# Performance work log

Measured on AMD Instinct MI355X. Metric: run time of the kernel, lower is better.

## Reference

```python
import jax, jax.numpy as jnp
import numpy as np

B, L, D, H, NB = 256, 200, 128, 4, 2
ITEMS = 50000
EPS = 1e-8
C = 0.001
REG = 0.0001


def _ln(x, g, b):
    m = x.mean(-1, keepdims=True)
    v = ((x - m) ** 2).mean(-1, keepdims=True)
    return (x - m) / jnp.sqrt(v + EPS) * g + b


def _mha(q_in, kv_in, in_w, in_b, out_w, out_b, mask):
    # q_in, kv_in: (B, L, D); torch MultiheadAttention math (batch-layout equivalent)
    Wq, Wk, Wv = jnp.split(in_w, 3, axis=0)
    bq, bk, bv = jnp.split(in_b, 3, axis=0)
    hd = D // H
    heads = lambda x: x.reshape(B, L, H, hd).transpose(0, 2, 1, 3)
    q = heads(q_in @ Wq.T + bq)
    k = heads(kv_in @ Wk.T + bk)
    v = heads(kv_in @ Wv.T + bv)
    scores = jnp.einsum('bhqd,bhkd->bhqk', q, k) * (1.0 / np.sqrt(hd))
    scores = jnp.where(mask, -jnp.inf, scores)
    a = jax.nn.softmax(scores, axis=-1)
    o = jnp.einsum('bhqk,bhkd->bhqd', a, v).transpose(0, 2, 1, 3).reshape(B, L, D)
    return o @ out_w.T + out_b


def _log2feats(log_seqs, item_emb, pos_emb, blocks):
    seqs = item_emb[log_seqs]                                   # (B,L,D)
    poss = jnp.arange(1, L + 1)[None, :] * (log_seqs != 0)      # 0 at padding
    seqs = seqs + pos_emb[poss]
    mask = ~jnp.tril(jnp.ones((L, L), dtype=bool))              # causal
    for i in range(NB):
        (ln1_g, ln1_b, in_w, in_b, out_w, out_b,
         ln2_g, ln2_b, c1_w, c1_b, c2_w, c2_b) = [p[i] for p in blocks]
        Q = _ln(seqs, ln1_g, ln1_b)
        seqs = Q + _mha(Q, seqs, in_w, in_b, out_w, out_b, mask)  # residual on Q (as in source)
        seqs = _ln(seqs, ln2_g, ln2_b)
        # PointWiseFeedForward: conv1d k=1 == linear over feature dim, residual add
        seqs = seqs + (jax.nn.relu(seqs @ c1_w.T + c1_b) @ c2_w.T + c2_b)
    return seqs


def setup_inputs() -> dict:
    key = jax.random.key(0)
    ks = jax.random.split(key, 20)
    inp = {
        'user_ids': jax.random.randint(ks[0], (B,), 0, 10000),
        'log_seqs': jax.random.randint(ks[1], (B, L), 0, ITEMS + 1),
        'pos_seqs': jax.random.randint(ks[2], (B, L), 0, ITEMS + 1),
        'item_emb': (jax.random.normal(ks[3], (ITEMS + 1, D)) * 0.02).at[0].set(0.0),
        'pos_emb': (jax.random.normal(ks[4], (L + 1, D)) * 0.02).at[0].set(0.0),
        'pred_w': jax.random.normal(ks[5], (1, D)) * 0.05,
        'ln1_g': jnp.ones((NB, D)), 'ln1_b': jnp.zeros((NB, D)),
        'in_w': jax.random.normal(ks[6], (NB, 3 * D, D)) * 0.05,
        'in_b': jnp.zeros((NB, 3 * D)),
        'out_w': jax.random.normal(ks[7], (NB, D, D)) * 0.05,
        'out_b': jnp.zeros((NB, D)),
        'ln2_g': jnp.ones((NB, D)), 'ln2_b': jnp.zeros((NB, D)),
        'c1_w': jax.random.normal(ks[8], (NB, D, D)) * 0.05,
        'c1_b': jnp.zeros((NB, D)),
        'c2_w': jax.random.normal(ks[9], (NB, D, D)) * 0.05,
        'c2_b': jnp.zeros((NB, D)),
    }
    return inp


def reference(user_ids, log_seqs, pos_seqs, item_emb, pos_emb, pred_w,
              ln1_g, ln1_b, in_w, in_b, out_w, out_b, ln2_g, ln2_b,
              c1_w, c1_b, c2_w, c2_b):
    blocks = (ln1_g, ln1_b, in_w, in_b, out_w, out_b, ln2_g, ln2_b, c1_w, c1_b, c2_w, c2_b)
    F = _log2feats(log_seqs, item_emb, pos_emb, blocks)          # (B,L,D)
    # left: FF = sum_s F F^T (per batch), EE = E^T E over full catalog, hh = w^T w
    FF = jnp.einsum('bsd,bse->bde', F, F)                        # (B,D,D)
    EE = item_emb.T @ item_emb                                   # (D,D)
    hh = pred_w.T @ pred_w                                       # (D,D)
    left = jnp.einsum('bde,ef,fg->b', FF, C * EE, hh)            # sum of FF @ cEE @ hh
    # right: R_hat = h^T (F * q_i)
    pos_e = item_emb[pos_seqs]                                   # (B,L,D)
    R = jnp.einsum('d,bsd->bs', pred_w[0], F * pos_e)
    right = ((1.0 - C) * R ** 2 - 2.0 * R).sum(axis=-1)
    reg = jnp.sqrt((item_emb ** 2).sum())                        # Frobenius norm
    loss = left + right + REG * reg
    return loss.mean()
```

## Files before the change

### kernel.cpp

```cpp
#include <hip/hip_runtime.h>
#include <math.h>

#define B_ 256
#define L_ 200
#define D_ 128
#define H_ 4
#define HD_ 32
#define NB_ 2
#define NROWS (B_ * L_)
#define NITEMS 50001
#define EPS_ 1e-8f
#define C_ 0.001f
#define REG_ 0.0001f

typedef __bf16 bf16x8 __attribute__((ext_vector_type(8)));
typedef short  short8 __attribute__((ext_vector_type(8)));
typedef float  f32x4  __attribute__((ext_vector_type(4)));
typedef unsigned short us4 __attribute__((ext_vector_type(4)));

static __device__ __forceinline__ void split2(float f, unsigned short& h, unsigned short& l) {
  unsigned u = __builtin_bit_cast(unsigned, f);
  unsigned hb = (u + 0x7FFFu + ((u >> 16) & 1u)) >> 16;
  float fl = f - __builtin_bit_cast(float, hb << 16);
  h = (unsigned short)hb;
  l = (unsigned short)(__builtin_bit_cast(unsigned, fl) >> 16);
}

static __device__ __forceinline__ bf16x8 pack8(const unsigned short* s) {
  short8 v;
#pragma unroll
  for (int j = 0; j < 8; ++j) v[j] = (short)s[j];
  return __builtin_bit_cast(bf16x8, v);
}

__global__ __launch_bounds__(256) void k_convw(const float* __restrict__ in_w,
                                               const float* __restrict__ out_w,
                                               const float* __restrict__ c1_w,
                                               const float* __restrict__ c2_w,
                                               unsigned short* __restrict__ Wh,
                                               unsigned short* __restrict__ Wl) {
  int i = (blockIdx.x * 256 + threadIdx.x) * 4;
  if (i >= 196608) return;
  const float* s; int j;
  if (i < 98304)       { s = in_w;  j = i; }
  else if (i < 131072) { s = out_w; j = i - 98304; }
  else if (i < 163840) { s = c1_w;  j = i - 131072; }
  else                 { s = c2_w;  j = i - 163840; }
  float4 v = *(const float4*)(s + j);
  float vf[4] = {v.x, v.y, v.z, v.w};
  us4 hv, lv;
#pragma unroll
  for (int t = 0; t < 4; ++t) {
    unsigned short h, l; split2(vf[t], h, l);
    hv[t] = h; lv[t] = l;
  }
  *(us4*)(Wh + i) = hv;
  *(us4*)(Wl + i) = lv;
}

__global__ __launch_bounds__(256) void k_embed(const int* __restrict__ logs,
                                               const float* __restrict__ item_emb,
                                               const float* __restrict__ pos_emb,
                                               float* __restrict__ X) {
  int gid = blockIdx.x * 256 + threadIdx.x;
  if (gid >= NROWS * 32) return;
  int row = gid >> 5;
  int c4  = (gid & 31) << 2;
  int it  = logs[row];
  int l   = row % L_;
  int pos = (it != 0) ? (l + 1) : 0;
  float4 e = *(const float4*)(item_emb + (size_t)it * D_ + c4);
  float4 p = *(const float4*)(pos_emb + (size_t)pos * D_ + c4);
  float4 o; o.x = e.x + p.x; o.y = e.y + p.y; o.z = e.z + p.z; o.w = e.w + p.w;
  *(float4*)(X + (size_t)row * D_ + c4) = o;
}

__global__ __launch_bounds__(256) void k_ln(const float* __restrict__ in,
                                            const float* __restrict__ g,
                                            const float* __restrict__ bb,
                                            float* __restrict__ out) {
  int wid = threadIdx.x >> 6, lane = threadIdx.x & 63;
  int row = blockIdx.x * 4 + wid;
  float2 x = *(const float2*)(in + (size_t)row * D_ + lane * 2);
  float s = x.x + x.y;
#pragma unroll
  for (int o = 1; o < 64; o <<= 1) s += __shfl_xor(s, o, 64);
  float m = s * (1.f / D_);
  float d0 = x.x - m, d1 = x.y - m;
  float ss = d0 * d0 + d1 * d1;
#pragma unroll
  for (int o = 1; o < 64; o <<= 1) ss += __shfl_xor(ss, o, 64);
  float rs = 1.f / sqrtf(ss * (1.f / D_) + EPS_);
  float2 gv = *(const float2*)(g + lane * 2);
  float2 bv = *(const float2*)(bb + lane * 2);
  float2 o2; o2.x = d0 * rs * gv.x + bv.x; o2.y = d1 * rs * gv.y + bv.y;
  *(float2*)(out + (size_t)row * D_ + lane * 2) = o2;
}

__global__ __launch_bounds__(256) void k_gemm2(const float* __restrict__ A, int lda,
                                               const unsigned short* __restrict__ Wh,
                                               const unsigned short* __restrict__ Wl,
                                               const float* __restrict__ bias,
                                               const float* __restrict__ Res,
                                               float* __restrict__ Cmat, int ldc,
                                               int col0, int epi) {
  Wh   += (size_t)blockIdx.y * 128 * 128;
  Wl   += (size_t)blockIdx.y * 128 * 128;
  bias += blockIdx.y * 128;
  col0 += blockIdx.y * 128;
  __shared__ unsigned short Ah[64][136], Al[64][136];
  const int tid  = threadIdx.x;
  const int bm   = blockIdx.x * 64;
  const int lane = tid & 63, wid = tid >> 6;
  const int n0   = wid * 32;
  const int fr   = lane & 15;
  const int fg   = lane >> 4;

  bf16x8 wh[2][4], wl[2][4];
#pragma unroll
  for (int f = 0; f < 2; f++)
#pragma unroll
    for (int ks = 0; ks < 4; ks++) {
      const unsigned short* p = Wh + (size_t)(n0 + f * 16 + fr) * 128 + ks * 32 + fg * 8;
      const unsigned short* q = Wl + (size_t)(n0 + f * 16 + fr) * 128 + ks * 32 + fg * 8;
      wh[f][ks] = __builtin_bit_cast(bf16x8, *(const short8*)p);
      wl[f][ks] = __builtin_bit_cast(bf16x8, *(const short8*)q);
    }

#pragma unroll
  for (int it = 0; it < 4; ++it) {
    int flat = it * 2048 + tid * 8;
    int r = flat >> 7, c = flat & 127;
    const float* ap = A + (size_t)(bm + r) * lda + c;
    float4 a0 = *(const float4*)ap;
    float4 a1 = *(const float4*)(ap + 4);
    float af[8] = {a0.x, a0.y, a0.z, a0.w, a1.x, a1.y, a1.z, a1.w};
    unsigned short hh[8], ll[8];
#pragma unroll
    for (int j = 0; j < 8; ++j) split2(af[j], hh[j], ll[j]);
    *(short8*)&Ah[r][c] = __builtin_bit_cast(short8, pack8(hh));
    *(short8*)&Al[r][c] = __builtin_bit_cast(short8, pack8(ll));
  }
  __syncthreads();

  f32x4 acc[4][2];
#pragma unroll
  for (int m = 0; m < 4; m++)
#pragma unroll
    for (int f = 0; f < 2; f++) acc[m][f] = (f32x4){0.f, 0.f, 0.f, 0.f};

#pragma unroll
  for (int m = 0; m < 4; m++) {
#pragma unroll
    for (int ks = 0; ks < 4; ks++) {
      bf16x8 ah = *(const bf16x8*)&Ah[m * 16 + fr][ks * 32 + fg * 8];
      bf16x8 al = *(const bf16x8*)&Al[m * 16 + fr][ks * 32 + fg * 8];
#pragma unroll
      for (int f = 0; f < 2; f++) {
        acc[m][f] = __builtin_amdgcn_mfma_f32_16x16x32_bf16(ah, wl[f][ks], acc[m][f], 0, 0, 0);
        acc[m][f] = __builtin_amdgcn_mfma_f32_16x16x32_bf16(al, wh[f][ks], acc[m][f], 0, 0, 0);
        acc[m][f] = __builtin_amdgcn_mfma_f32_16x16x32_bf16(ah, wh[f][ks], acc[m][f], 0, 0, 0);
      }
    }
  }

#pragma unroll
  for (int f = 0; f < 2; f++) {
    int n = n0 + f * 16 + fr;
    float bv = bias[n];
#pragma unroll
    for (int m = 0; m < 4; m++) {
#pragma unroll
      for (int i = 0; i < 4; i++) {
        int row = bm + m * 16 + fg * 4 + i;
        float v = acc[m][f][i] + bv;
        if (epi == 2)      v = fmaxf(v, 0.f);
        else if (epi == 1) v += Res[(size_t)row * D_ + n];
        Cmat[(size_t)row * ldc + col0 + n] = v;
      }
    }
  }
}

__global__ __launch_bounds__(256) void k_attn(const float* __restrict__ qkv,
                                              float* __restrict__ Oq) {
  __shared__ float ks[L_][HD_];
  __shared__ float vs[L_][HD_];
  int b = blockIdx.x >> 2;
  int h = blockIdx.x & 3;
  int tid = threadIdx.x;
  for (int idx = tid; idx < L_ * HD_; idx += 256) {
    int j = idx >> 5, d = idx & 31;
    size_t base = ((size_t)(b * L_ + j)) * 384 + 128 + h * HD_ + d;
    ks[j][d] = qkv[base];
    vs[j][d] = qkv[base + 128];
  }
  __syncthreads();
  int t = tid;
  if (t >= L_) return;
  float q[HD_];
  const float* qp = qkv + ((size_t)(b * L_ + t)) * 384 + h * HD_;
#pragma unroll
  for (int d4 = 0; d4 < HD_; d4 += 4) {
    float4 v = *(const float4*)(qp + d4);
    q[d4] = v.x; q[d4 + 1] = v.y; q[d4 + 2] = v.z; q[d4 + 3] = v.w;
  }
  float o[HD_];
#pragma unroll
  for (int d = 0; d < HD_; d++) o[d] = 0.f;
  float mrun = -INFINITY, lrun = 0.f;
  const float scale = 0.17677669529663687f;
  for (int j = 0; j <= t; j++) {
    float s = 0.f;
#pragma unroll
    for (int d = 0; d < HD_; d++) s += q[d] * ks[j][d];
    s *= scale;
    float mn = fmaxf(mrun, s);
    float corr = __expf(mrun - mn);
    float p = __expf(s - mn);
    lrun = lrun * corr + p;
#pragma unroll
    for (int d = 0; d < HD_; d++) o[d] = o[d] * corr + p * vs[j][d];
    mrun = mn;
  }
  float inv = 1.f / lrun;
  float* op = Oq + ((size_t)(b * L_ + t)) * 384 + h * HD_;
#pragma unroll
  for (int d4 = 0; d4 < HD_; d4 += 4) {
    float4 v;
    v.x = o[d4] * inv; v.y = o[d4 + 1] * inv;
    v.z = o[d4 + 2] * inv; v.w = o[d4 + 3] * inv;
    *(float4*)(op + d4) = v;
  }
}

__global__ void k_zero(float* __restrict__ w_raw, float* __restrict__ reg_sq) {
  int t = threadIdx.x;
  if (t < 128) w_raw[t] = 0.f;
  if (t == 128) reg_sq[0] = 0.f;
}

__global__ __launch_bounds__(256) void k_wreg(const float* __restrict__ item_emb,
                                              const float* __restrict__ pred_w,
                                              float* __restrict__ w_raw,
                                              float* __restrict__ reg_sq) {
  int gw = (blockIdx.x * 256 + threadIdx.x) >> 6;
  int lane = threadIdx.x & 63;
  float2 p2 = *(const float2*)(pred_w + lane * 2);
  float ax = 0.f, ay = 0.f, ssq = 0.f;
  for (int r = gw; r < NITEMS; r += 1024) {
    float2 e = *(const float2*)(item_emb + (size_t)r * D_ + lane * 2);
    float dp = e.x * p2.x + e.y * p2.y;
#pragma unroll
    for (int o = 1; o < 64; o <<= 1) dp += __shfl_xor(dp, o, 64);
    ax += e.x * dp; ay += e.y * dp;
    ssq += e.x * e.x + e.y * e.y;
  }
  atomicAdd(&w_raw[lane * 2 + 0], ax);
  atomicAdd(&w_raw[lane * 2 + 1], ay);
#pragma unroll
  for (int o = 1; o < 64; o <<= 1) ssq += __shfl_xor(ssq, o, 64);
  if (lane == 0) atomicAdd(reg_sq, ssq);
}

__global__ void k_scale(const float* __restrict__ pred_w,
                        const float* __restrict__ w_raw,
                        const float* __restrict__ reg_sq,
                        float* __restrict__ wt, float* __restrict__ out) {
  int t = threadIdx.x;
  __shared__ float sp[128];
  sp[t] = pred_w[t];
  __syncthreads();
  float S = 0.f;
  for (int i = 0; i < 128; i++) S += sp[i];
  wt[t] = C_ * S * w_raw[t];
  if (t == 0) out[0] = REG_ * sqrtf(reg_sq[0]);
}

__global__ __launch_bounds__(256) void k_final(const float* __restrict__ F,
                                               const int* __restrict__ pos_seqs,
                                               const float* __restrict__ item_emb,
                                               const float* __restrict__ pred_w,
                                               const float* __restrict__ wt,
                                               float* __restrict__ out) {
  int b = blockIdx.x;
  int wid = threadIdx.x >> 6, lane = threadIdx.x & 63;
  float2 wt2 = *(const float2*)(wt + lane * 2);
  float2 p2  = *(const float2*)(pred_w + lane * 2);
  float acc = 0.f;
  for (int s = wid; s < L_; s += 4) {
    float2 f = *(const float2*)(F + ((size_t)(b * L_ + s)) * D_ + lane * 2);
    int pi = pos_seqs[b * L_ + s];
    float2 pe = *(const float2*)(item_emb + (size_t)pi * D_ + lane * 2);
    float rsum = f.x + f.y;
    float dw = f.x * wt2.x + f.y * wt2.y;
    float rr = p2.x * f.x * pe.x + p2.y * f.y * pe.y;
#pragma unroll
    for (int o = 1; o < 64; o <<= 1) {
      rsum += __shfl_xor(rsum, o, 64);
      dw   += __shfl_xor(dw, o, 64);
      rr   += __shfl_xor(rr, o, 64);
    }
    acc += rsum * dw + (1.f - C_) * rr * rr - 2.f * rr;
  }
  if (lane == 0) atomicAdd(out, acc * (1.f / B_));
}

extern "C" void kernel_launch(void* const* d_in, const int* in_sizes, int n_in,
                              void* d_out, int out_size, void* d_ws, size_t ws_size,
                              hipStream_t stream) {
  const int*   log_seqs = (const int*)d_in[1];
  const int*   pos_seqs = (const int*)d_in[2];
  const float* item_emb = (const float*)d_in[3];
  const float* pos_emb  = (const float*)d_in[4];
  const float* pred_w   = (const float*)d_in[5];
  const float* ln1_g = (const float*)d_in[6];
  const float* ln1_b = (const float*)d_in[7];
  const float* in_w  = (const float*)d_in[8];
  const float* in_b  = (const float*)d_in[9];
  const float* out_w = (const float*)d_in[10];
  const float* out_b = (const float*)d_in[11];
  const float* ln2_g = (const float*)d_in[12];
  const float* ln2_b = (const float*)d_in[13];
  const float* c1_w  = (const float*)d_in[14];
  const float* c1_b  = (const float*)d_in[15];
  const float* c2_w  = (const float*)d_in[16];
  const float* c2_b  = (const float*)d_in[17];
  float* out = (float*)d_out;

  char* ws = (char*)d_ws;
  const size_t UNIT = (size_t)NROWS * D_ * sizeof(float);
  float* X     = (float*)ws; ws += UNIT;
  float* QB    = (float*)ws; ws += UNIT;
  float* QKV   = (float*)ws; ws += 3 * UNIT;
  unsigned short* WH = (unsigned short*)ws; ws += 196608 * 2;
  unsigned short* WL = (unsigned short*)ws; ws += 196608 * 2;
  float* w_raw = (float*)ws; ws += 512;
  float* wt    = (float*)ws; ws += 512;
  float* reg_sq= (float*)ws; ws += 512;
  if (ws_size < 5 * UNIT + 4 * 196608 + 4096) return;

  const size_t OFF_OUT = 98304, OFF_C1 = 131072, OFF_C2 = 163840;

  k_zero<<<1, 256, 0, stream>>>(w_raw, reg_sq);
  k_convw<<<192, 256, 0, stream>>>(in_w, out_w, c1_w, c2_w, WH, WL);
  k_embed<<<(NROWS * 32) / 256, 256, 0, stream>>>(log_seqs, item_emb, pos_emb, X);

  for (int i = 0; i < NB_; i++) {
    const size_t iwo = (size_t)i * 384 * 128;
    const size_t sqo = (size_t)i * 128 * 128;
    const float* ib = in_b + (size_t)i * 384;
    k_ln<<<NROWS / 4, 256, 0, stream>>>(X, ln1_g + i * 128, ln1_b + i * 128, QB);
    k_gemm2<<<dim3(NROWS / 64, 1), 256, 0, stream>>>(QB, 128, WH + iwo, WL + iwo,
                                                     ib, nullptr, QKV, 384, 0, 0);
    k_gemm2<<<dim3(NROWS / 64, 2), 256, 0, stream>>>(X, 128, WH + iwo + 128 * 128,
                                                     WL + iwo + 128 * 128,
                                                     ib + 128, nullptr, QKV, 384, 128, 0);
    k_attn<<<B_ * H_, 256, 0, stream>>>(QKV, QKV);
    k_gemm2<<<dim3(NROWS / 64, 1), 256, 0, stream>>>(QKV, 384, WH + OFF_OUT + sqo,
                                                     WL + OFF_OUT + sqo,
                                                     out_b + i * 128, QB, X, 128, 0, 1);
    k_ln<<<NROWS / 4, 256, 0, stream>>>(X, ln2_g + i * 128, ln2_b + i * 128, QB);
    k_gemm2<<<dim3(NROWS / 64, 1), 256, 0, stream>>>(QB, 128, WH + OFF_C1 + sqo,
                                                     WL + OFF_C1 + sqo,
                                                     c1_b + i * 128, nullptr, QKV, 128, 0, 2);
    k_gemm2<<<dim3(NROWS / 64, 1), 256, 0, stream>>>(QKV, 128, WH + OFF_C2 + sqo,
                                                     WL + OFF_C2 + sqo,
                                                     c2_b + i * 128, QB, X, 128, 0, 1);
  }

  k_wreg<<<256, 256, 0, stream>>>(item_emb, pred_w, w_raw, reg_sq);
  k_scale<<<1, 128, 0, stream>>>(pred_w, w_raw, reg_sq, wt, out);
  k_final<<<B_, 256, 0, stream>>>(X, pos_seqs, item_emb, pred_w, wt, out);
}
```

Baseline: 786.9 us.

## Rewrite causal attention with split-bf16 MFMA for QK^T and PV

Replaces the per-thread scalar online-softmax attention with a wave-tiled version. K and V are split into bf16 hi/lo pairs in shared memory, with V stored transposed. Scores and the P·V product are computed with three-term 16x16x32 bf16 MFMAs, and softmax runs over causal 16-row tiles using wave shuffles. This removes the scalar FMA-bound inner loop and the load imbalance across causal rows, at the cost of extra split/shuffle work and some precision loss from dropping the lo*lo term.

```diff
diff --git a/kernel.cpp b/kernel.cpp
--- a/kernel.cpp
+++ b/kernel.cpp
@@ -5,13 +5,14 @@
 #define L_ 200
 #define D_ 128
 #define H_ 4
-#define HD_ 32
 #define NB_ 2
 #define NROWS (B_ * L_)
 #define NITEMS 50001
 #define EPS_ 1e-8f
 #define C_ 0.001f
 #define REG_ 0.0001f
+#define KPADK_ 208
+#define KPADV_ 224
 
 typedef __bf16 bf16x8 __attribute__((ext_vector_type(8)));
 typedef short  short8 __attribute__((ext_vector_type(8)));
@@ -182,55 +183,137 @@
   }
 }
 
-__global__ __launch_bounds__(256) void k_attn(const float* __restrict__ qkv,
-                                              float* __restrict__ Oq) {
-  __shared__ float ks[L_][HD_];
-  __shared__ float vs[L_][HD_];
-  int b = blockIdx.x >> 2;
-  int h = blockIdx.x & 3;
-  int tid = threadIdx.x;
-  for (int idx = tid; idx < L_ * HD_; idx += 256) {
-    int j = idx >> 5, d = idx & 31;
-    size_t base = ((size_t)(b * L_ + j)) * 384 + 128 + h * HD_ + d;
-    ks[j][d] = qkv[base];
-    vs[j][d] = qkv[base + 128];
+__global__ __launch_bounds__(256) void k_attn2(const float* __restrict__ qkv,
+                                               float* __restrict__ Oq) {
+  __shared__ unsigned short Kh[KPADK_][32], Kl[KPADK_][32];
+  __shared__ unsigned short Vh[32][KPADV_], Vl[32][KPADV_];
+  const int b = blockIdx.x >> 2, h = blockIdx.x & 3;
+  const int tid = threadIdx.x, lane = tid & 63, w = tid >> 6;
+  const size_t rb = (size_t)b * L_;
+
+#pragma unroll
+  for (int it = 0; it < 13; ++it) {
+    int e = it * 256 + tid;
+    int r = e >> 4;
+    int d2 = (e & 15) * 2;
+    int src = r < L_ ? r : L_ - 1;
+    const float* kp = qkv + (rb + src) * 384 + 128 + h * 32 + d2;
+    float2 kv2 = *(const float2*)kp;
+    unsigned short h0, l0, h1, l1;
+    split2(kv2.x, h0, l0); split2(kv2.y, h1, l1);
+    *(unsigned*)&Kh[r][d2] = (unsigned)h0 | ((unsigned)h1 << 16);
+    *(unsigned*)&Kl[r][d2] = (unsigned)l0 | ((unsigned)l1 << 16);
+  }
+#pragma unroll
+  for (int it = 0; it < 14; ++it) {
+    int e = it * 256 + tid;
+    int d = e & 31, k = (e >> 5) * 2;
+    float v0 = (k     < L_) ? qkv[(rb + k    ) * 384 + 256 + h * 32 + d] : 0.f;
+    float v1 = (k + 1 < L_) ? qkv[(rb + k + 1) * 384 + 256 + h * 32 + d] : 0.f;
+    unsigned short h0, l0, h1, l1;
+    split2(v0, h0, l0); split2(v1, h1, l1);
+    *(unsigned*)&Vh[d][k] = (unsigned)h0 | ((unsigned)h1 << 16);
+    *(unsigned*)&Vl[d][k] = (unsigned)l0 | ((unsigned)l1 << 16);
   }
   __syncthreads();
-  int t = tid;
-  if (t >= L_) return;
-  float q[HD_];
-  const float* qp = qkv + ((size_t)(b * L_ + t)) * 384 + h * HD_;
-#pragma unroll
-  for (int d4 = 0; d4 < HD_; d4 += 4) {
-    float4 v = *(const float4*)(qp + d4);
-    q[d4] = v.x; q[d4 + 1] = v.y; q[d4 + 2] = v.z; q[d4 + 3] = v.w;
-  }
-  float o[HD_];
-#pragma unroll
-  for (int d = 0; d < HD_; d++) o[d] = 0.f;
-  float mrun = -INFINITY, lrun = 0.f;
+
   const float scale = 0.17677669529663687f;
-  for (int j = 0; j <= t; j++) {
-    float s = 0.f;
-#pragma unroll
-    for (int d = 0; d < HD_; d++) s += q[d] * ks[j][d];
-    s *= scale;
-    float mn = fmaxf(mrun, s);
-    float corr = __expf(mrun - mn);
-    float p = __expf(s - mn);
-    lrun = lrun * corr + p;
-#pragma unroll
-    for (int d = 0; d < HD_; d++) o[d] = o[d] * corr + p * vs[j][d];
-    mrun = mn;
-  }
-  float inv = 1.f / lrun;
-  float* op = Oq + ((size_t)(b * L_ + t)) * 384 + h * HD_;
-#pragma unroll
-  for (int d4 = 0; d4 < HD_; d4 += 4) {
-    float4 v;
-    v.x = o[d4] * inv; v.y = o[d4 + 1] * inv;
-    v.z = o[d4 + 2] * inv; v.w = o[d4 + 3] * inv;
-    *(float4*)(op + d4) = v;
+  const int fr = lane & 15, g = lane >> 4;
+  f32x4 ps[14];
+#pragma unroll
+  for (int t = 0; t < 14; ++t) ps[t] = (f32x4){0.f, 0.f, 0.f, 0.f};
+
+  for (int qi = 0; qi < 4; ++qi) {
+    int qt = w + qi * 4;
+    if (qt >= 13) break;
+    const int ntiles = qt + 1;
+    const int q = qt * 16 + fr;
+    int qsrc = q < L_ ? q : L_ - 1;
+    const float* qp = qkv + (rb + qsrc) * 384 + h * 32 + g * 8;
+    float4 q0 = *(const float4*)qp, q1 = *(const float4*)(qp + 4);
+    float qf[8] = {q0.x, q0.y, q0.z, q0.w, q1.x, q1.y, q1.z, q1.w};
+    unsigned short qh_[8], ql_[8];
+#pragma unroll
+    for (int j = 0; j < 8; ++j) split2(qf[j], qh_[j], ql_[j]);
+    bf16x8 qh = pack8(qh_), ql = pack8(ql_);
+
+#pragma unroll
+    for (int kt = 0; kt < 13; ++kt) {
+      if (kt > qt) break;
+      bf16x8 kh = *(const bf16x8*)&Kh[kt * 16 + fr][g * 8];
+      bf16x8 kl = *(const bf16x8*)&Kl[kt * 16 + fr][g * 8];
+      f32x4 s = (f32x4){0.f, 0.f, 0.f, 0.f};
+      s = __builtin_amdgcn_mfma_f32_16x16x32_bf16(kh, ql, s, 0, 0, 0);
+      s = __builtin_amdgcn_mfma_f32_16x16x32_bf16(kl, qh, s, 0, 0, 0);
+      s = __builtin_amdgcn_mfma_f32_16x16x32_bf16(kh, qh, s, 0, 0, 0);
+#pragma unroll
+      for (int i = 0; i < 4; ++i) {
+        int k = kt * 16 + g * 4 + i;
+        ps[kt][i] = (k <= q && k < L_) ? s[i] * scale : -1e30f;
+      }
+    }
+    float m = -1e30f;
+#pragma unroll
+    for (int kt = 0; kt < 13; ++kt) {
+      if (kt > qt) break;
+      m = fmaxf(m, fmaxf(fmaxf(ps[kt][0], ps[kt][1]), fmaxf(ps[kt][2], ps[kt][3])));
+    }
+    m = fmaxf(m, __shfl_xor(m, 16, 64));
+    m = fmaxf(m, __shfl_xor(m, 32, 64));
+    float lsum = 0.f;
+#pragma unroll
+    for (int kt = 0; kt < 13; ++kt) {
+      if (kt > qt) break;
+#pragma unroll
+      for (int i = 0; i < 4; ++i) {
+        float p = __expf(ps[kt][i] - m);
+        ps[kt][i] = p;
+        lsum += p;
+      }
+    }
+    lsum += __shfl_xor(lsum, 16, 64);
+    lsum += __shfl_xor(lsum, 32, 64);
+    float rcp = 1.f / lsum;
+    float linv[4];
+#pragma unroll
+    for (int i = 0; i < 4; ++i) linv[i] = __shfl(rcp, 4 * g + i, 64);
+
+    const int npairs = (ntiles + 1) >> 1;
+    f32x4 o0 = (f32x4){0.f, 0.f, 0.f, 0.f};
+    f32x4 o1 = (f32x4){0.f, 0.f, 0.f, 0.f};
+#pragma unroll
+    for (int p = 0; p < 7; ++p) {
+      if (p >= npairs) break;
+      unsigned short pha[8], pla[8];
+#pragma unroll
+      for (int j = 0; j < 8; ++j) {
+        int src = fr + 32 * ((lane >> 4) & 1) + 16 * (j >> 2);
+        float v0 = __shfl(ps[2 * p][j & 3], src, 64);
+        float v1 = __shfl(ps[2 * p + 1][j & 3], src, 64);
+        float v = (lane >= 32) ? v1 : v0;
+        split2(v, pha[j], pla[j]);
+      }
+      bf16x8 pah = pack8(pha), pal = pack8(pla);
+      bf16x8 vh0 = *(const bf16x8*)&Vh[fr][p * 32 + g * 8];
+      bf16x8 vl0 = *(const bf16x8*)&Vl[fr][p * 32 + g * 8];
+      bf16x8 vh1 = *(const bf16x8*)&Vh[16 + fr][p * 32 + g * 8];
+      bf16x8 vl1 = *(const bf16x8*)&Vl[16 + fr][p * 32 + g * 8];
+      o0 = __builtin_amdgcn_mfma_f32_16x16x32_bf16(pah, vl0, o0, 0, 0, 0);
+      o0 = __builtin_amdgcn_mfma_f32_16x16x32_bf16(pal, vh0, o0, 0, 0, 0);
+      o0 = __builtin_amdgcn_mfma_f32_16x16x32_bf16(pah, vh0, o0, 0, 0, 0);
+      o1 = __builtin_amdgcn_mfma_f32_16x16x32_bf16(pah, vl1, o1, 0, 0, 0);
+      o1 = __builtin_amdgcn_mfma_f32_16x16x32_bf16(pal, vh1, o1, 0, 0, 0);
+      o1 = __builtin_amdgcn_mfma_f32_16x16x32_bf16(pah, vh1, o1, 0, 0, 0);
+    }
+#pragma unroll
+    for (int i = 0; i < 4; ++i) {
+      int qrow = qt * 16 + 4 * g + i;
+      if (qrow < L_) {
+        float* op = Oq + (rb + qrow) * 384 + h * 32;
+        op[fr]      = o0[i] * linv[i];
+        op[16 + fr] = o1[i] * linv[i];
+      }
+    }
   }
 }
 
@@ -356,7 +439,7 @@
     k_gemm2<<<dim3(NROWS / 64, 2), 256, 0, stream>>>(X, 128, WH + iwo + 128 * 128,
                                                      WL + iwo + 128 * 128,
                                                      ib + 128, nullptr, QKV, 384, 128, 0);
-    k_attn<<<B_ * H_, 256, 0, stream>>>(QKV, QKV);
+    k_attn2<<<B_ * H_, 256, 0, stream>>>(QKV, QKV);
     k_gemm2<<<dim3(NROWS / 64, 1), 256, 0, stream>>>(QKV, 384, WH + OFF_OUT + sqo,
                                                      WL + OFF_OUT + sqo,
                                                      out_b + i * 128, QB, X, 128, 0, 1);
```

After: 688.2 us. 1.14x faster.
